# Kernel optimization log

Hardware: AMD Instinct MI355X
Metric: run time of the kernel (lower is better)

The kernel has to match this reference:

```python
import jax, jax.numpy as jnp
import numpy as np

EPS = 1e-12

def l2_normalize(x):
    # matches torch.nn.functional.normalize(p=2): x / max(||x||, eps)
    n = jnp.sqrt(jnp.sum(x * x, axis=-1, keepdims=True))
    return x / jnp.maximum(n, EPS)

def setup_inputs() -> dict:
    key = jax.random.key(0)
    k1, k2, k3, k4 = jax.random.split(key, 4)
    batch, n_neg, E, n_rel = 512, 2048, 256, 1000
    return {
        "head_emb": jax.random.normal(k1, (batch, E), dtype=jnp.float32),
        "tail_emb": jax.random.normal(k2, (1, n_neg, E), dtype=jnp.float32),
        "relation_embedding": jax.random.normal(k3, (n_rel, 2 * E), dtype=jnp.float32),
        "relation_id": jax.random.randint(k4, (batch,), 0, n_rel, dtype=jnp.int64),
    }

def reference(head_emb, tail_emb, relation_embedding, relation_id):
    # PairRE.score_tails with negative_sample_sharing=True, scoring_norm=2,
    # normalize_entities=True.
    E = head_emb.shape[-1]
    rel = relation_embedding[relation_id]          # (batch, 2E)
    r_h, r_t = rel[:, :E], rel[:, E:]              # (batch, E) each
    h = l2_normalize(head_emb)                     # (batch, E)
    t = l2_normalize(tail_emb)                     # (1, n_neg, E)
    t = t.reshape(1, -1, E)                        # negative sample sharing
    # diff: (batch, n_neg, E)
    diff = t * r_t[:, None, :] - (h * r_h)[:, None, :]
    # p=2 norm reduction over embedding dim -> (batch, n_neg)
    return -jnp.sqrt(jnp.sum(diff * diff, axis=-1))
```

## Files before the change

### kernel.cpp

```cpp
#include <hip/hip_runtime.h>
#include <hip/hip_bf16.h>


#define B_DIM 512
#define N_DIM 2048
#define E_DIM 256
#define K_DIM 512
#define NSTEP 16
#define FRAG_US 512

typedef __attribute__((ext_vector_type(8))) __bf16 bf16x8;
typedef __attribute__((ext_vector_type(4))) float f32x4;

__device__ inline ushort f2bf(float x) {
    __hip_bfloat16 h = __float2bfloat16(x);
    union { __hip_bfloat16 b; ushort u; } cv; cv.b = h; return cv.u;
}

__device__ inline float wave_sum(float v) {
#pragma unroll
    for (int m = 1; m < 64; m <<= 1) v += __shfl_xor(v, m, 64);
    return v;
}

__global__ __launch_bounds__(256) void prep_kernel(
        const float* __restrict__ head, const float* __restrict__ tail,
        const float* __restrict__ rel,  const int* __restrict__ rid,
        ushort* __restrict__ Tbig, ushort* __restrict__ Abig,
        float* __restrict__ cvec) {
    const int tid = threadIdx.x, lane = tid & 63, wv = tid >> 6;
    const int w = blockIdx.x * 4 + wv;
    const int s_ = lane >> 2, q = lane & 3;
    const int k0 = lane * 8;
    const bool sqr = (k0 < E_DIM);
    const int e0 = k0 & (E_DIM - 1);

    if (w < N_DIM) {
        const int n = w;
        const float* row = tail + (size_t)n * E_DIM;
        const float4 v4 = ((const float4*)row)[lane];
        const float s = wave_sum(v4.x * v4.x + v4.y * v4.y + v4.z * v4.z + v4.w * v4.w);
        const float inv = 1.0f / fmaxf(sqrtf(s), 1e-12f);
        const float4 f0 = *(const float4*)(row + e0);
        const float4 f1 = *(const float4*)(row + e0 + 4);
        const float v[8] = {f0.x, f0.y, f0.z, f0.w, f1.x, f1.y, f1.z, f1.w};
        ushort u[8];
#pragma unroll
        for (int j = 0; j < 8; ++j) {
            float x = v[j] * inv;
            if (sqr) x *= x;
            u[j] = f2bf(x);
        }
        const int g = n >> 4, m = n & 15;
        *(uint4*)(Tbig + (size_t)((g * 16 + s_) * 64 + q * 16 + m) * 8) = *(const uint4*)u;
    } else {
        const int b = w - N_DIM;
        const int id = rid[b];
        const float* hrow  = head + (size_t)b * E_DIM;
        const float* rhrow = rel + (size_t)id * (2 * E_DIM);
        const float* rtrow = rhrow + E_DIM;
        const float4 h4  = ((const float4*)hrow)[lane];
        const float4 rh4 = ((const float4*)rhrow)[lane];
        const float s1 = wave_sum(h4.x * h4.x + h4.y * h4.y + h4.z * h4.z + h4.w * h4.w);
        const float inv = 1.0f / fmaxf(sqrtf(s1), 1e-12f);
        const float p0 = h4.x * inv * rh4.x, p1 = h4.y * inv * rh4.y;
        const float p2 = h4.z * inv * rh4.z, p3 = h4.w * inv * rh4.w;
        const float s2 = wave_sum(p0 * p0 + p1 * p1 + p2 * p2 + p3 * p3);
        if (lane == 0) cvec[b] = s2;

        const float4 rt0 = *(const float4*)(rtrow + e0);
        const float4 rt1 = *(const float4*)(rtrow + e0 + 4);
        const float rt[8] = {rt0.x, rt0.y, rt0.z, rt0.w, rt1.x, rt1.y, rt1.z, rt1.w};
        float v[8];
        if (sqr) {
#pragma unroll
            for (int j = 0; j < 8; ++j) v[j] = rt[j] * rt[j];
        } else {
            const float4 h0 = *(const float4*)(hrow + e0);
            const float4 h1 = *(const float4*)(hrow + e0 + 4);
            const float4 r0 = *(const float4*)(rhrow + e0);
            const float4 r1 = *(const float4*)(rhrow + e0 + 4);
            const float hh[8] = {h0.x, h0.y, h0.z, h0.w, h1.x, h1.y, h1.z, h1.w};
            const float rr[8] = {r0.x, r0.y, r0.z, r0.w, r1.x, r1.y, r1.z, r1.w};
#pragma unroll
            for (int j = 0; j < 8; ++j) v[j] = -2.0f * rt[j] * (hh[j] * inv * rr[j]);
        }
        ushort u[8];
#pragma unroll
        for (int j = 0; j < 8; ++j) u[j] = f2bf(v[j]);
        const int g = b >> 4, m = b & 15;
        *(uint4*)(Abig + (size_t)((g * 16 + s_) * 64 + q * 16 + m) * 8) = *(const uint4*)u;
    }
}

__global__ __launch_bounds__(256) void score_kernel(
        const ushort* __restrict__ Tbig, const ushort* __restrict__ Abig,
        const float* __restrict__ cvec, float* __restrict__ out) {
    const int tid = threadIdx.x, lane = tid & 63, wv = tid >> 6;
    const int p_n = blockIdx.x, b_super = blockIdx.y;
    const int gA  = b_super * 2 + (wv & 1);
    const int gT0 = p_n * 4 + (wv >> 1) * 2;

    const ushort* Ab  = Abig + (size_t)gA * NSTEP * FRAG_US + lane * 8;
    const ushort* Tb0 = Tbig + (size_t)gT0 * NSTEP * FRAG_US + lane * 8;
    const ushort* Tb1 = Tb0 + (size_t)NSTEP * FRAG_US;

    f32x4 acc0 = {0.f, 0.f, 0.f, 0.f}, acc1 = {0.f, 0.f, 0.f, 0.f};

    bf16x8 a_c  = *(const bf16x8*)(Ab);
    bf16x8 b0_c = *(const bf16x8*)(Tb0);
    bf16x8 b1_c = *(const bf16x8*)(Tb1);
#pragma unroll
    for (int s = 0; s < NSTEP - 1; ++s) {
        const bf16x8 a_n  = *(const bf16x8*)(Ab  + (s + 1) * FRAG_US);
        const bf16x8 b0_n = *(const bf16x8*)(Tb0 + (s + 1) * FRAG_US);
        const bf16x8 b1_n = *(const bf16x8*)(Tb1 + (s + 1) * FRAG_US);
        acc0 = __builtin_amdgcn_mfma_f32_16x16x32_bf16(a_c, b0_c, acc0, 0, 0, 0);
        acc1 = __builtin_amdgcn_mfma_f32_16x16x32_bf16(a_c, b1_c, acc1, 0, 0, 0);
        a_c = a_n; b0_c = b0_n; b1_c = b1_n;
    }
    acc0 = __builtin_amdgcn_mfma_f32_16x16x32_bf16(a_c, b0_c, acc0, 0, 0, 0);
    acc1 = __builtin_amdgcn_mfma_f32_16x16x32_bf16(a_c, b1_c, acc1, 0, 0, 0);

    const int ml = lane & 15, q = lane >> 4;
    const int b0 = gA * 16;
    const int n0 = gT0 * 16;
#pragma unroll
    for (int r = 0; r < 4; ++r) {
        const int b = b0 + q * 4 + r;
        const float cb = cvec[b];
        out[(size_t)b * N_DIM + n0 + ml]      = -sqrtf(fmaxf(acc0[r] + cb, 0.f));
        out[(size_t)b * N_DIM + n0 + 16 + ml] = -sqrtf(fmaxf(acc1[r] + cb, 0.f));
    }
}

__device__ inline float block_reduce_sum_256(float v, float* buf) {
#pragma unroll
    for (int o = 32; o > 0; o >>= 1) v += __shfl_down(v, o, 64);
    const int lane = threadIdx.x & 63, wid = threadIdx.x >> 6;
    __syncthreads();
    if (lane == 0) buf[wid] = v;
    __syncthreads();
    return buf[0] + buf[1] + buf[2] + buf[3];
}

__global__ __launch_bounds__(256) void fallback_kernel(
        const float* __restrict__ head, const float* __restrict__ tail,
        const float* __restrict__ rel,  const int* __restrict__ rid,
        float* __restrict__ out) {
    __shared__ float Hh[E_DIM];
    __shared__ float RT[E_DIM];
    __shared__ float buf[4];
    const int b = blockIdx.x;
    const int tid = threadIdx.x;
    const float hv = head[(size_t)b * E_DIM + tid];
    const int id = rid[b];
    const float rh = rel[(size_t)id * (2 * E_DIM) + tid];
    const float rt = rel[(size_t)id * (2 * E_DIM) + E_DIM + tid];
    const float tot = block_reduce_sum_256(hv * hv, buf);
    const float inv = 1.0f / fmaxf(sqrtf(tot), 1e-12f);
    const float HhV = hv * inv * rh;
    Hh[tid] = HhV; RT[tid] = rt;
    const float c = block_reduce_sum_256(HhV * HhV, buf);
    __syncthreads();
    for (int n = tid; n < N_DIM; n += 256) {
        float S1 = 0.f, S2 = 0.f, Stt = 0.f;
        for (int e = 0; e < E_DIM; ++e) {
            const float tv = tail[(size_t)n * E_DIM + e];
            const float p = tv * RT[e];
            S1 += p * p; S2 += p * Hh[e]; Stt += tv * tv;
        }
        const float al = 1.0f / fmaxf(sqrtf(Stt), 1e-12f);
        const float x = al * al * S1 - 2.0f * al * S2 + c;
        out[(size_t)b * N_DIM + n] = -sqrtf(fmaxf(x, 0.f));
    }
}

extern "C" void kernel_launch(void* const* d_in, const int* in_sizes, int n_in,
                              void* d_out, int out_size, void* d_ws, size_t ws_size,
                              hipStream_t stream) {
    const float* head = (const float*)d_in[0];
    const float* tail = (const float*)d_in[1];
    const float* rel  = (const float*)d_in[2];
    const int*   rid  = (const int*)d_in[3];
    float* out = (float*)d_out;

    const size_t needT = (size_t)N_DIM * K_DIM * sizeof(ushort);
    const size_t needA = (size_t)B_DIM * K_DIM * sizeof(ushort);
    const size_t needC = (size_t)B_DIM * sizeof(float);
    if (ws_size >= needT + needA + needC) {
        ushort* Tbig = (ushort*)d_ws;
        ushort* Abig = Tbig + (size_t)N_DIM * K_DIM;
        float*  cvec = (float*)(Abig + (size_t)B_DIM * K_DIM);
        prep_kernel<<<(N_DIM + B_DIM) / 4, 256, 0, stream>>>(head, tail, rel, rid,
                                                             Tbig, Abig, cvec);
        dim3 grid(N_DIM / 64, B_DIM / 32);
        score_kernel<<<grid, 256, 0, stream>>>(Tbig, Abig, cvec, out);
    } else {
        fallback_kernel<<<B_DIM, 256, 0, stream>>>(head, tail, rel, rid, out);
    }
}
```

Measured before the change: 68.46 us.

## Fuse prep and scoring into one cooperative kernel with a grid sync

Replaces the two kernel launches with one cooperative launch of 256 blocks. Each wave preprocesses up to three rows, then a grid-wide barrier separates that phase from scoring. The scoring tile is also enlarged so each wave computes a 32x32 output block with four MFMA accumulators, reusing both A and T fragments. This removes one launch and its gap, at the cost of fewer waves in flight and the expense of the grid barrier. It also drops the workspace-size check and the fp32 fallback kernel.

```diff
diff --git a/kernel.cpp b/kernel.cpp
--- a/kernel.cpp
+++ b/kernel.cpp
@@ -1,5 +1,6 @@
 #include <hip/hip_runtime.h>
 #include <hip/hip_bf16.h>
+#include <hip/hip_cooperative_groups.h>
 
 
 #define B_DIM 512
@@ -8,6 +9,8 @@
 #define K_DIM 512
 #define NSTEP 16
 #define FRAG_US 512
+
+namespace cg = cooperative_groups;
 
 typedef __attribute__((ext_vector_type(8))) __bf16 bf16x8;
 typedef __attribute__((ext_vector_type(4))) float f32x4;
@@ -23,13 +26,11 @@
     return v;
 }
 
-__global__ __launch_bounds__(256) void prep_kernel(
+__device__ inline void prep_row(int w, int lane,
         const float* __restrict__ head, const float* __restrict__ tail,
         const float* __restrict__ rel,  const int* __restrict__ rid,
         ushort* __restrict__ Tbig, ushort* __restrict__ Abig,
         float* __restrict__ cvec) {
-    const int tid = threadIdx.x, lane = tid & 63, wv = tid >> 6;
-    const int w = blockIdx.x * 4 + wv;
     const int s_ = lane >> 2, q = lane & 3;
     const int k0 = lane * 8;
     const bool sqr = (k0 < E_DIM);
@@ -93,87 +94,84 @@
     }
 }
 
+__device__ inline void score_tile(int g, int lane,
+        const ushort* __restrict__ Tbig, const ushort* __restrict__ Abig,
+        const float* __restrict__ cvec, float* __restrict__ out) {
+    const int p_b = g >> 6, p_n = g & 63;
+    const ushort* A0 = Abig + (size_t)(p_b * 2) * NSTEP * FRAG_US + lane * 8;
+    const ushort* A1 = A0 + (size_t)NSTEP * FRAG_US;
+    const ushort* T0 = Tbig + (size_t)(p_n * 2) * NSTEP * FRAG_US + lane * 8;
+    const ushort* T1 = T0 + (size_t)NSTEP * FRAG_US;
+
+    f32x4 acc00 = {0,0,0,0}, acc01 = {0,0,0,0}, acc10 = {0,0,0,0}, acc11 = {0,0,0,0};
+
+    bf16x8 a0 = *(const bf16x8*)(A0);
+    bf16x8 a1 = *(const bf16x8*)(A1);
+    bf16x8 t0 = *(const bf16x8*)(T0);
+    bf16x8 t1 = *(const bf16x8*)(T1);
+#pragma unroll
+    for (int s = 0; s < NSTEP - 1; ++s) {
+        const bf16x8 a0n = *(const bf16x8*)(A0 + (s + 1) * FRAG_US);
+        const bf16x8 a1n = *(const bf16x8*)(A1 + (s + 1) * FRAG_US);
+        const bf16x8 t0n = *(const bf16x8*)(T0 + (s + 1) * FRAG_US);
+        const bf16x8 t1n = *(const bf16x8*)(T1 + (s + 1) * FRAG_US);
+        acc00 = __builtin_amdgcn_mfma_f32_16x16x32_bf16(a0, t0, acc00, 0, 0, 0);
+        acc01 = __builtin_amdgcn_mfma_f32_16x16x32_bf16(a0, t1, acc01, 0, 0, 0);
+        acc10 = __builtin_amdgcn_mfma_f32_16x16x32_bf16(a1, t0, acc10, 0, 0, 0);
+        acc11 = __builtin_amdgcn_mfma_f32_16x16x32_bf16(a1, t1, acc11, 0, 0, 0);
+        a0 = a0n; a1 = a1n; t0 = t0n; t1 = t1n;
+    }
+    acc00 = __builtin_amdgcn_mfma_f32_16x16x32_bf16(a0, t0, acc00, 0, 0, 0);
+    acc01 = __builtin_amdgcn_mfma_f32_16x16x32_bf16(a0, t1, acc01, 0, 0, 0);
+    acc10 = __builtin_amdgcn_mfma_f32_16x16x32_bf16(a1, t0, acc10, 0, 0, 0);
+    acc11 = __builtin_amdgcn_mfma_f32_16x16x32_bf16(a1, t1, acc11, 0, 0, 0);
+
+    const int ml = lane & 15, q = lane >> 4;
+    const int bb0 = p_b * 32, nn0 = p_n * 32;
+#pragma unroll
+    for (int r = 0; r < 4; ++r) {
+        const int b_lo = bb0 + q * 4 + r;
+        const int b_hi = b_lo + 16;
+        const float cb_lo = cvec[b_lo];
+        const float cb_hi = cvec[b_hi];
+        out[(size_t)b_lo * N_DIM + nn0 + ml]      = -sqrtf(fmaxf(acc00[r] + cb_lo, 0.f));
+        out[(size_t)b_lo * N_DIM + nn0 + 16 + ml] = -sqrtf(fmaxf(acc01[r] + cb_lo, 0.f));
+        out[(size_t)b_hi * N_DIM + nn0 + ml]      = -sqrtf(fmaxf(acc10[r] + cb_hi, 0.f));
+        out[(size_t)b_hi * N_DIM + nn0 + 16 + ml] = -sqrtf(fmaxf(acc11[r] + cb_hi, 0.f));
+    }
+}
+
+__global__ __launch_bounds__(256) void pairre_coop(
+        const float* __restrict__ head, const float* __restrict__ tail,
+        const float* __restrict__ rel,  const int* __restrict__ rid,
+        ushort* __restrict__ Tbig, ushort* __restrict__ Abig,
+        float* __restrict__ cvec, float* __restrict__ out) {
+    const int lane = threadIdx.x & 63, wv = threadIdx.x >> 6;
+    const int gw = blockIdx.x * 4 + wv;
+    prep_row(gw, lane, head, tail, rel, rid, Tbig, Abig, cvec);
+    prep_row(gw + 1024, lane, head, tail, rel, rid, Tbig, Abig, cvec);
+    if (gw < 512)
+        prep_row(gw + 2048, lane, head, tail, rel, rid, Tbig, Abig, cvec);
+
+    cg::this_grid().sync();
+
+    score_tile(gw, lane, Tbig, Abig, cvec, out);
+}
+
+__global__ __launch_bounds__(256) void prep_kernel(
+        const float* __restrict__ head, const float* __restrict__ tail,
+        const float* __restrict__ rel,  const int* __restrict__ rid,
+        ushort* __restrict__ Tbig, ushort* __restrict__ Abig,
+        float* __restrict__ cvec) {
+    const int lane = threadIdx.x & 63, wv = threadIdx.x >> 6;
+    prep_row(blockIdx.x * 4 + wv, lane, head, tail, rel, rid, Tbig, Abig, cvec);
+}
+
 __global__ __launch_bounds__(256) void score_kernel(
         const ushort* __restrict__ Tbig, const ushort* __restrict__ Abig,
         const float* __restrict__ cvec, float* __restrict__ out) {
-    const int tid = threadIdx.x, lane = tid & 63, wv = tid >> 6;
-    const int p_n = blockIdx.x, b_super = blockIdx.y;
-    const int gA  = b_super * 2 + (wv & 1);
-    const int gT0 = p_n * 4 + (wv >> 1) * 2;
-
-    const ushort* Ab  = Abig + (size_t)gA * NSTEP * FRAG_US + lane * 8;
-    const ushort* Tb0 = Tbig + (size_t)gT0 * NSTEP * FRAG_US + lane * 8;
-    const ushort* Tb1 = Tb0 + (size_t)NSTEP * FRAG_US;
-
-    f32x4 acc0 = {0.f, 0.f, 0.f, 0.f}, acc1 = {0.f, 0.f, 0.f, 0.f};
-
-    bf16x8 a_c  = *(const bf16x8*)(Ab);
-    bf16x8 b0_c = *(const bf16x8*)(Tb0);
-    bf16x8 b1_c = *(const bf16x8*)(Tb1);
-#pragma unroll
-    for (int s = 0; s < NSTEP - 1; ++s) {
-        const bf16x8 a_n  = *(const bf16x8*)(Ab  + (s + 1) * FRAG_US);
-        const bf16x8 b0_n = *(const bf16x8*)(Tb0 + (s + 1) * FRAG_US);
-        const bf16x8 b1_n = *(const bf16x8*)(Tb1 + (s + 1) * FRAG_US);
-        acc0 = __builtin_amdgcn_mfma_f32_16x16x32_bf16(a_c, b0_c, acc0, 0, 0, 0);
-        acc1 = __builtin_amdgcn_mfma_f32_16x16x32_bf16(a_c, b1_c, acc1, 0, 0, 0);
-        a_c = a_n; b0_c = b0_n; b1_c = b1_n;
-    }
-    acc0 = __builtin_amdgcn_mfma_f32_16x16x32_bf16(a_c, b0_c, acc0, 0, 0, 0);
-    acc1 = __builtin_amdgcn_mfma_f32_16x16x32_bf16(a_c, b1_c, acc1, 0, 0, 0);
-
-    const int ml = lane & 15, q = lane >> 4;
-    const int b0 = gA * 16;
-    const int n0 = gT0 * 16;
-#pragma unroll
-    for (int r = 0; r < 4; ++r) {
-        const int b = b0 + q * 4 + r;
-        const float cb = cvec[b];
-        out[(size_t)b * N_DIM + n0 + ml]      = -sqrtf(fmaxf(acc0[r] + cb, 0.f));
-        out[(size_t)b * N_DIM + n0 + 16 + ml] = -sqrtf(fmaxf(acc1[r] + cb, 0.f));
-    }
-}
-
-__device__ inline float block_reduce_sum_256(float v, float* buf) {
-#pragma unroll
-    for (int o = 32; o > 0; o >>= 1) v += __shfl_down(v, o, 64);
-    const int lane = threadIdx.x & 63, wid = threadIdx.x >> 6;
-    __syncthreads();
-    if (lane == 0) buf[wid] = v;
-    __syncthreads();
-    return buf[0] + buf[1] + buf[2] + buf[3];
-}
-
-__global__ __launch_bounds__(256) void fallback_kernel(
-        const float* __restrict__ head, const float* __restrict__ tail,
-        const float* __restrict__ rel,  const int* __restrict__ rid,
-        float* __restrict__ out) {
-    __shared__ float Hh[E_DIM];
-    __shared__ float RT[E_DIM];
-    __shared__ float buf[4];
-    const int b = blockIdx.x;
-    const int tid = threadIdx.x;
-    const float hv = head[(size_t)b * E_DIM + tid];
-    const int id = rid[b];
-    const float rh = rel[(size_t)id * (2 * E_DIM) + tid];
-    const float rt = rel[(size_t)id * (2 * E_DIM) + E_DIM + tid];
-    const float tot = block_reduce_sum_256(hv * hv, buf);
-    const float inv = 1.0f / fmaxf(sqrtf(tot), 1e-12f);
-    const float HhV = hv * inv * rh;
-    Hh[tid] = HhV; RT[tid] = rt;
-    const float c = block_reduce_sum_256(HhV * HhV, buf);
-    __syncthreads();
-    for (int n = tid; n < N_DIM; n += 256) {
-        float S1 = 0.f, S2 = 0.f, Stt = 0.f;
-        for (int e = 0; e < E_DIM; ++e) {
-            const float tv = tail[(size_t)n * E_DIM + e];
-            const float p = tv * RT[e];
-            S1 += p * p; S2 += p * Hh[e]; Stt += tv * tv;
-        }
-        const float al = 1.0f / fmaxf(sqrtf(Stt), 1e-12f);
-        const float x = al * al * S1 - 2.0f * al * S2 + c;
-        out[(size_t)b * N_DIM + n] = -sqrtf(fmaxf(x, 0.f));
-    }
+    const int lane = threadIdx.x & 63, wv = threadIdx.x >> 6;
+    score_tile(blockIdx.x * 4 + wv, lane, Tbig, Abig, cvec, out);
 }
 
 extern "C" void kernel_launch(void* const* d_in, const int* in_sizes, int n_in,
@@ -185,18 +183,16 @@
     const int*   rid  = (const int*)d_in[3];
     float* out = (float*)d_out;
 
-    const size_t needT = (size_t)N_DIM * K_DIM * sizeof(ushort);
-    const size_t needA = (size_t)B_DIM * K_DIM * sizeof(ushort);
-    const size_t needC = (size_t)B_DIM * sizeof(float);
-    if (ws_size >= needT + needA + needC) {
-        ushort* Tbig = (ushort*)d_ws;
-        ushort* Abig = Tbig + (size_t)N_DIM * K_DIM;
-        float*  cvec = (float*)(Abig + (size_t)B_DIM * K_DIM);
-        prep_kernel<<<(N_DIM + B_DIM) / 4, 256, 0, stream>>>(head, tail, rel, rid,
-                                                             Tbig, Abig, cvec);
-        dim3 grid(N_DIM / 64, B_DIM / 32);
-        score_kernel<<<grid, 256, 0, stream>>>(Tbig, Abig, cvec, out);
-    } else {
-        fallback_kernel<<<B_DIM, 256, 0, stream>>>(head, tail, rel, rid, out);
+    ushort* Tbig = (ushort*)d_ws;
+    ushort* Abig = Tbig + (size_t)N_DIM * K_DIM;
+    float*  cvec = (float*)(Abig + (size_t)B_DIM * K_DIM);
+
+    void* args[] = { (void*)&head, (void*)&tail, (void*)&rel, (void*)&rid,
+                     (void*)&Tbig, (void*)&Abig, (void*)&cvec, (void*)&out };
+    hipError_t e = hipLaunchCooperativeKernel((const void*)pairre_coop,
+                                              dim3(256), dim3(256), args, 0, stream);
+    if (e != hipSuccess) {
+        prep_kernel<<<640, 256, 0, stream>>>(head, tail, rel, rid, Tbig, Abig, cvec);
+        score_kernel<<<256, 256, 0, stream>>>(Tbig, Abig, cvec, out);
     }
 }
```

After: 116.2 us. 1.7x slower.
